# Optimization experiments

Measured on AMD Instinct MI355X. Metric: run time of the kernel, lower is better.

Reference implementation:

```python
import jax, jax.numpy as jnp
import numpy as np

D_K = 64  # module-level constant in source
NEG = -1e9


def setup_inputs() -> dict:
    key = jax.random.key(0)
    k1, k2, k3, k4 = jax.random.split(key, 4)
    B, H, S, D = 4, 16, 2048, 64
    query = jax.random.normal(k1, (B, H, S, D), dtype=jnp.float32)
    key_t = jax.random.normal(k2, (B, H, S, D), dtype=jnp.float32)
    value = jax.random.normal(k3, (B, H, S, D), dtype=jnp.float32)
    mask = jax.random.randint(k4, (B, 1, S, S), 0, 2) == 1  # bool, broadcast over heads
    return {"query": query, "key": key_t, "value": value, "mask": mask}


def reference(query, key, value, mask):
    # scores = QK^T / sqrt(d_k)   [B,H,S,S]
    scores = jnp.einsum("bhqd,bhkd->bhqk", query, key) / jnp.sqrt(jnp.float32(D_K))
    # masked_fill_(mask, -1e9)
    scores = jnp.where(mask, jnp.float32(NEG), scores)
    # non-standard: multiply masked scores by V, then log_softmax over last dim
    out = jnp.einsum("bhqk,bhkd->bhqd", scores, value)  # [B,H,S,d_v]
    return jax.nn.log_softmax(out, axis=-1)
```

## Files before the change

### kernel.cpp

```cpp
#include <hip/hip_runtime.h>
#include <hip/hip_bf16.h>


typedef __attribute__((ext_vector_type(8))) short bf16x8;
typedef __attribute__((ext_vector_type(16))) float f32x16;

#define NEGV (-1e9f)

__device__ inline unsigned cvt_bf16(float f) {
    unsigned u = __builtin_bit_cast(unsigned, f);
    u += 0x7FFFu + ((u >> 16) & 1u);
    return u >> 16;
}
__device__ inline unsigned pk_bf16(float a, float b) {
    return cvt_bf16(a) | (cvt_bf16(b) << 16);
}
__device__ inline unsigned pk_trunc(float a, float b) {
    return __builtin_amdgcn_perm(__builtin_bit_cast(unsigned, b),
                                 __builtin_bit_cast(unsigned, a), 0x07060302u);
}

__global__ __launch_bounds__(256)
void mask_pack(const int* __restrict__ M, unsigned long long* __restrict__ bitT) {
    const int lane = threadIdx.x & 63;
    const int gw   = (blockIdx.x * 256 + threadIdx.x) >> 6;
    const int nw   = (gridDim.x * 256) >> 6;
    for (int w = gw; w < 4 * 8 * 32 * 256; w += nw) {
        const int q  = w & 255;
        const int ki = (w >> 8) & 31;
        const int qt = (w >> 13) & 7;
        const int b  = w >> 16;
        const int m  = M[((size_t)(b * 2048 + qt * 256 + q)) * 2048 + ki * 64 + lane];
        const unsigned long long bal = __ballot(m != 0);
        if (lane == 0) bitT[w] = bal;
    }
}

__global__ __launch_bounds__(256, 4)
void attn_kernel(const float* __restrict__ Q, const float* __restrict__ K,
                 const float* __restrict__ V,
                 const unsigned long long* __restrict__ bitT,
                 float* __restrict__ Out) {
    __shared__ __attribute__((aligned(16))) unsigned short sK[2][64 * 72];
    __shared__ __attribute__((aligned(16))) unsigned short sVt[2][64 * 72];

    const int tid  = threadIdx.x;
    const int wave = tid >> 6;
    const int lane = tid & 63;
    const int half = lane >> 5;
    const int l32  = lane & 31;

    const int bid = blockIdx.x;
    const int h   = bid & 15;
    const int qt2 = (bid >> 4) & 15;
    const int b   = bid >> 8;
    const int bh  = b * 16 + h;
    const int q0  = qt2 * 128;
    const int qt  = qt2 >> 1;
    const int qh  = qt2 & 1;

    const float* Qb = Q + (size_t)(bh * 2048 + q0) * 64;
    const float* Kb = K + (size_t)bh * 2048 * 64;
    const float* Vb = V + (size_t)bh * 2048 * 64;
    const unsigned long long* Bt = bitT + (size_t)(b * 8 + qt) * 32 * 256
                                 + qh * 128 + wave * 32 + l32;

    float4 kp[4];
    float  vp[16];
    unsigned long long mw = Bt[0];
    const int krow = tid >> 4, kc4 = tid & 15;
#pragma unroll
    for (int i = 0; i < 4; i++)
        kp[i] = *(const float4*)(Kb + (size_t)(krow + i * 16) * 64 + kc4 * 4);
#pragma unroll
    for (int i = 0; i < 2; i++) {
        const int kb = (wave * 2 + i) * 8;
#pragma unroll
        for (int j = 0; j < 8; j++)
            vp[i * 8 + j] = Vb[(size_t)(kb + j) * 64 + lane];
    }

    bf16x8 qF[4];
    {
        const float* qr = Qb + (size_t)(wave * 32 + l32) * 64 + half * 8;
#pragma unroll
        for (int dk = 0; dk < 4; dk++) {
            const float4 f0 = *(const float4*)(qr + dk * 16);
            const float4 f1 = *(const float4*)(qr + dk * 16 + 4);
            union { bf16x8 v; unsigned u[4]; } t;
            t.u[0] = pk_bf16(f0.x * 0.125f, f0.y * 0.125f);
            t.u[1] = pk_bf16(f0.z * 0.125f, f0.w * 0.125f);
            t.u[2] = pk_bf16(f1.x * 0.125f, f1.y * 0.125f);
            t.u[3] = pk_bf16(f1.z * 0.125f, f1.w * 0.125f);
            qF[dk] = t.v;
        }
    }

    f32x16 Oacc[2];
#pragma unroll
    for (int db = 0; db < 2; db++)
#pragma unroll
        for (int r = 0; r < 16; r++) Oacc[db][r] = 0.f;

    for (int ki = 0; ki < 32; ki++) {
        const int cur = ki & 1;

#pragma unroll
        for (int i = 0; i < 4; i++) {
            uint2 p;
            p.x = pk_trunc(kp[i].x, kp[i].y);
            p.y = pk_trunc(kp[i].z, kp[i].w);
            *(uint2*)&sK[cur][(krow + i * 16) * 72 + kc4 * 4] = p;
        }
#pragma unroll
        for (int i = 0; i < 2; i++) {
            const int kb = (wave * 2 + i) * 8;
            uint4 p4;
            p4.x = pk_bf16(vp[i * 8 + 0], vp[i * 8 + 1]);
            p4.y = pk_bf16(vp[i * 8 + 2], vp[i * 8 + 3]);
            p4.z = pk_bf16(vp[i * 8 + 4], vp[i * 8 + 5]);
            p4.w = pk_bf16(vp[i * 8 + 6], vp[i * 8 + 7]);
            *(uint4*)&sVt[cur][lane * 72 + kb] = p4;
        }

        __syncthreads();

        unsigned long long mwN = 0;
        if (ki < 31) {
            const int kn = (ki + 1) * 64;
            mwN = Bt[(ki + 1) * 256];
#pragma unroll
            for (int i = 0; i < 4; i++)
                kp[i] = *(const float4*)(Kb + (size_t)(kn + krow + i * 16) * 64 + kc4 * 4);
#pragma unroll
            for (int i = 0; i < 2; i++) {
                const int kb = (wave * 2 + i) * 8;
#pragma unroll
                for (int j = 0; j < 8; j++)
                    vp[i * 8 + j] = Vb[(size_t)(kn + kb + j) * 64 + lane];
            }
        }

#pragma unroll
        for (int jk = 0; jk < 2; jk++) {
            bf16x8 aK[4];
#pragma unroll
            for (int dk = 0; dk < 4; dk++)
                aK[dk] = *(const bf16x8*)&sK[cur][(jk * 32 + l32) * 72 + dk * 16 + half * 8];
            bf16x8 bV[2][2];
#pragma unroll
            for (int p = 0; p < 2; p++)
#pragma unroll
                for (int db = 0; db < 2; db++)
                    bV[p][db] = *(const bf16x8*)&sVt[cur][(db * 32 + l32) * 72 + (jk * 2 + p) * 16 + half * 8];

            const unsigned b32 = (unsigned)(mw >> (jk * 32));
            const unsigned bsh = b32 >> (half * 4);

            f32x16 acc;
#pragma unroll
            for (int rg = 0; rg < 4; rg++) {
                const unsigned nib = bsh >> (rg * 8);
                acc[rg * 4 + 0] = (nib & 1u) ? NEGV : 0.f;
                acc[rg * 4 + 1] = (nib & 2u) ? NEGV : 0.f;
                acc[rg * 4 + 2] = (nib & 4u) ? NEGV : 0.f;
                acc[rg * 4 + 3] = (nib & 8u) ? NEGV : 0.f;
            }
#pragma unroll
            for (int dk = 0; dk < 4; dk++)
                acc = __builtin_amdgcn_mfma_f32_32x32x16_bf16(aK[dk], qF[dk], acc, 0, 0, 0);

#pragma unroll
            for (int p = 0; p < 2; p++) {
                const unsigned P0 = pk_trunc(acc[p * 8 + 0], acc[p * 8 + 1]);
                const unsigned P1 = pk_trunc(acc[p * 8 + 2], acc[p * 8 + 3]);
                const unsigned P2 = pk_trunc(acc[p * 8 + 4], acc[p * 8 + 5]);
                const unsigned P3 = pk_trunc(acc[p * 8 + 6], acc[p * 8 + 7]);
                auto r02 = __builtin_amdgcn_permlane32_swap(P0, P2, false, false);
                auto r13 = __builtin_amdgcn_permlane32_swap(P1, P3, false, false);
                union { bf16x8 v; unsigned u[4]; } aS;
                aS.u[0] = (unsigned)r02[0];
                aS.u[1] = (unsigned)r13[0];
                aS.u[2] = (unsigned)r02[1];
                aS.u[3] = (unsigned)r13[1];
#pragma unroll
                for (int db = 0; db < 2; db++)
                    Oacc[db] = __builtin_amdgcn_mfma_f32_32x32x16_bf16(aS.v, bV[p][db], Oacc[db], 0, 0, 0);
            }
        }

        mw = mwN;
    }

    float* Ob = Out + (size_t)bh * 2048 * 64;
#pragma unroll
    for (int r = 0; r < 16; r++) {
        const float v0 = Oacc[0][r], v1 = Oacc[1][r];
        float mx = fmaxf(v0, v1);
#pragma unroll
        for (int off = 1; off < 32; off <<= 1)
            mx = fmaxf(mx, __shfl_xor(mx, off, 64));
        float s = __expf(v0 - mx) + __expf(v1 - mx);
#pragma unroll
        for (int off = 1; off < 32; off <<= 1)
            s += __shfl_xor(s, off, 64);
        const float lse = mx + __logf(s);
        const int qrow = q0 + wave * 32 + (r & 3) + 8 * (r >> 2) + 4 * half;
        Ob[(size_t)qrow * 64 + l32]      = v0 - lse;
        Ob[(size_t)qrow * 64 + 32 + l32] = v1 - lse;
    }
}

extern "C" void kernel_launch(void* const* d_in, const int* in_sizes, int n_in,
                              void* d_out, int out_size, void* d_ws, size_t ws_size,
                              hipStream_t stream) {
    const float* Q = (const float*)d_in[0];
    const float* K = (const float*)d_in[1];
    const float* V = (const float*)d_in[2];
    const int*   M = (const int*)d_in[3];
    float* Out = (float*)d_out;
    unsigned long long* bitT = (unsigned long long*)d_ws;

    mask_pack<<<dim3(4096), dim3(256), 0, stream>>>(M, bitT);
    attn_kernel<<<dim3(1024), dim3(256), 0, stream>>>(Q, K, V, bitT, Out);
}
```

Before: 265.4 us.

## Use hardware bf16 pack convert, restructure mask packing, raise MFMA wave priority

```diff
diff --git a/kernel.cpp b/kernel.cpp
--- a/kernel.cpp
+++ b/kernel.cpp
@@ -7,13 +7,10 @@
 
 #define NEGV (-1e9f)
 
-__device__ inline unsigned cvt_bf16(float f) {
-    unsigned u = __builtin_bit_cast(unsigned, f);
-    u += 0x7FFFu + ((u >> 16) & 1u);
-    return u >> 16;
-}
-__device__ inline unsigned pk_bf16(float a, float b) {
-    return cvt_bf16(a) | (cvt_bf16(b) << 16);
+__device__ inline unsigned pk_cvt(float a, float b) {
+    unsigned r;
+    asm("v_cvt_pk_bf16_f32 %0, %1, %2" : "=v"(r) : "v"(a), "v"(b));
+    return r;
 }
 __device__ inline unsigned pk_trunc(float a, float b) {
     return __builtin_amdgcn_perm(__builtin_bit_cast(unsigned, b),
@@ -24,15 +21,16 @@
 void mask_pack(const int* __restrict__ M, unsigned long long* __restrict__ bitT) {
     const int lane = threadIdx.x & 63;
     const int gw   = (blockIdx.x * 256 + threadIdx.x) >> 6;
-    const int nw   = (gridDim.x * 256) >> 6;
-    for (int w = gw; w < 4 * 8 * 32 * 256; w += nw) {
-        const int q  = w & 255;
-        const int ki = (w >> 8) & 31;
-        const int qt = (w >> 13) & 7;
-        const int b  = w >> 16;
-        const int m  = M[((size_t)(b * 2048 + qt * 256 + q)) * 2048 + ki * 64 + lane];
+    const int b    = gw >> 11;
+    const int qt   = (gw >> 8) & 7;
+    const int q    = gw & 255;
+    const size_t mbase = (size_t)gw * 2048;
+    unsigned long long* dst = bitT + (size_t)(b * 8 + qt) * 32 * 256 + q;
+#pragma unroll 4
+    for (int ki = 0; ki < 32; ki++) {
+        const int m = M[mbase + ki * 64 + lane];
         const unsigned long long bal = __ballot(m != 0);
-        if (lane == 0) bitT[w] = bal;
+        if (lane == 0) dst[ki * 256] = bal;
     }
 }
 
@@ -88,10 +86,10 @@
             const float4 f0 = *(const float4*)(qr + dk * 16);
             const float4 f1 = *(const float4*)(qr + dk * 16 + 4);
             union { bf16x8 v; unsigned u[4]; } t;
-            t.u[0] = pk_bf16(f0.x * 0.125f, f0.y * 0.125f);
-            t.u[1] = pk_bf16(f0.z * 0.125f, f0.w * 0.125f);
-            t.u[2] = pk_bf16(f1.x * 0.125f, f1.y * 0.125f);
-            t.u[3] = pk_bf16(f1.z * 0.125f, f1.w * 0.125f);
+            t.u[0] = pk_cvt(f0.x * 0.125f, f0.y * 0.125f);
+            t.u[1] = pk_cvt(f0.z * 0.125f, f0.w * 0.125f);
+            t.u[2] = pk_cvt(f1.x * 0.125f, f1.y * 0.125f);
+            t.u[3] = pk_cvt(f1.z * 0.125f, f1.w * 0.125f);
             qF[dk] = t.v;
         }
     }
@@ -116,10 +114,10 @@
         for (int i = 0; i < 2; i++) {
             const int kb = (wave * 2 + i) * 8;
             uint4 p4;
-            p4.x = pk_bf16(vp[i * 8 + 0], vp[i * 8 + 1]);
-            p4.y = pk_bf16(vp[i * 8 + 2], vp[i * 8 + 3]);
-            p4.z = pk_bf16(vp[i * 8 + 4], vp[i * 8 + 5]);
-            p4.w = pk_bf16(vp[i * 8 + 6], vp[i * 8 + 7]);
+            p4.x = pk_cvt(vp[i * 8 + 0], vp[i * 8 + 1]);
+            p4.y = pk_cvt(vp[i * 8 + 2], vp[i * 8 + 3]);
+            p4.z = pk_cvt(vp[i * 8 + 4], vp[i * 8 + 5]);
+            p4.w = pk_cvt(vp[i * 8 + 6], vp[i * 8 + 7]);
             *(uint4*)&sVt[cur][lane * 72 + kb] = p4;
         }
 
@@ -166,6 +164,8 @@
                 acc[rg * 4 + 2] = (nib & 4u) ? NEGV : 0.f;
                 acc[rg * 4 + 3] = (nib & 8u) ? NEGV : 0.f;
             }
+
+            __builtin_amdgcn_s_setprio(1);
 #pragma unroll
             for (int dk = 0; dk < 4; dk++)
                 acc = __builtin_amdgcn_mfma_f32_32x32x16_bf16(aK[dk], qF[dk], acc, 0, 0, 0);
@@ -187,6 +187,7 @@
                 for (int db = 0; db < 2; db++)
                     Oacc[db] = __builtin_amdgcn_mfma_f32_32x32x16_bf16(aS.v, bV[p][db], Oacc[db], 0, 0, 0);
             }
+            __builtin_amdgcn_s_setprio(0);
         }
 
         mw = mwN;
@@ -221,6 +222,6 @@
     float* Out = (float*)d_out;
     unsigned long long* bitT = (unsigned long long*)d_ws;
 
-    mask_pack<<<dim3(4096), dim3(256), 0, stream>>>(M, bitT);
+    mask_pack<<<dim3(2048), dim3(256), 0, stream>>>(M, bitT);
     attn_kernel<<<dim3(1024), dim3(256), 0, stream>>>(Q, K, V, bitT, Out);
 }
```

Result: slower. 414.8 us (+56.3%).
